# Optimization experiments

Hardware: AMD Instinct MI355X
Metric: run time of the kernel (lower is better)

The kernel has to match this reference:

```python
import jax, jax.numpy as jnp
import numpy as np

B, N, D, H, DA, DL = 8, 1024, 512, 8, 64, 64
U_DIM = DL * H * 3          # 1536: u channel (3 attention channels worth)
NB = 128                    # timestamp-delta buckets
HID = 4 * D                 # FFN hidden (ffn_multiply=4)
EPS = 1e-6


def _rms(x):
    return x * jax.lax.rsqrt(jnp.mean(x * x, axis=-1, keepdims=True) + EPS)


def setup_inputs() -> dict:
    key = jax.random.key(0)
    ks = jax.random.split(key, 12)
    L = N // 2
    total = B * L
    x_offsets = jnp.arange(B + 1, dtype=jnp.int32) * L
    x = jax.random.normal(ks[0], (total, D), jnp.float32)
    all_timestamps = jnp.sort(jax.random.randint(ks[1], (B, N), 0, 1_000_000, dtype=jnp.int64), axis=1)
    invalid_attn_mask = jnp.tril(jnp.ones((N, N), jnp.float32))
    uvqk = jax.random.normal(ks[2], (D, DL * H * 4 + DA * H * 2), jnp.float32) * 0.02
    pos_w = jax.random.normal(ks[3], (2 * N - 1,), jnp.float32) * 0.02
    ts_w = jax.random.normal(ks[4], (NB,), jnp.float32) * 0.02
    W0 = jax.random.normal(ks[5], (U_DIM, D), jnp.float32) * (1.0 / np.sqrt(U_DIM))
    b0 = jnp.zeros((D,), jnp.float32)
    W1 = jax.random.normal(ks[6], (D, HID), jnp.float32) * (1.0 / np.sqrt(D))
    W2 = jax.random.normal(ks[7], (HID, D), jnp.float32) * (1.0 / np.sqrt(HID))
    W3 = jax.random.normal(ks[8], (D, HID), jnp.float32) * (1.0 / np.sqrt(D))
    return dict(x=x, x_offsets=x_offsets, all_timestamps=all_timestamps,
                invalid_attn_mask=invalid_attn_mask, uvqk=uvqk, pos_w=pos_w,
                ts_w=ts_w, W0=W0, b0=b0, W1=W1, W2=W2, W3=W3)


def reference(x, x_offsets, all_timestamps, invalid_attn_mask, uvqk, pos_w, ts_w, W0, b0, W1, W2, W3):
    total = x.shape[0]
    tok = jnp.arange(total)
    b_idx = jnp.searchsorted(x_offsets, tok, side='right') - 1   # batch id per jagged token
    p_idx = tok - x_offsets[b_idx]                               # position within sequence

    # input RMSNorm + fused uvqk projection with SiLU
    normed = _rms(x)
    mm = jax.nn.silu(normed @ uvqk)
    u, v, q, k = jnp.split(mm, [U_DIM, U_DIM + DL * H, U_DIM + DL * H + DA * H], axis=1)

    def pad(vals):  # jagged_to_padded_dense
        return jnp.zeros((B, N, vals.shape[-1]), vals.dtype).at[b_idx, p_idx].set(vals)

    pq = pad(q).reshape(B, N, H, DA)
    pk = pad(k).reshape(B, N, H, DA)
    pv = pad(v).reshape(B, N, H, DL)

    # channel 1: content-content SiLU attention
    qk_attn = jax.nn.silu(jnp.einsum('bnhd,bmhd->bhnm', pq, pk)) / N
    qk_attn = qk_attn * invalid_attn_mask[None, None]

    # channel 2: relative positional bias (shared across batch)
    rel = jnp.arange(N)[:, None] - jnp.arange(N)[None, :] + (N - 1)
    pos_attn = pos_w[rel] * invalid_attn_mask                     # (N, N)

    # channel 3: log-bucketed relative temporal bias
    dt = all_timestamps[:, :, None] - all_timestamps[:, None, :]
    bucket = jnp.clip(jnp.floor(jnp.log(jnp.abs(dt).astype(jnp.float32) + 1.0)).astype(jnp.int32), 0, NB - 1)
    ts_attn = ts_w[bucket] * invalid_attn_mask[None]              # (B, N, N)

    out_pos = jnp.einsum('nm,bmhd->bnhd', pos_attn, pv)
    out_ts = jnp.einsum('bnm,bmhd->bnhd', ts_attn, pv)
    out_lat = jnp.einsum('bhnm,bmhd->bnhd', qk_attn, pv)
    combined = jnp.concatenate([out_pos, out_ts, out_lat], axis=-1).reshape(B, N, U_DIM)
    attn_output = combined[b_idx, p_idx]                          # dense_to_jagged

    # AMS gating + multistage FFN with residuals
    ams = u * _rms(attn_output)
    X = ams @ W0 + b0 + x
    nX = _rms(X)
    X1 = jax.nn.silu(nX @ W1) * (nX @ W3)
    return X1 @ W2 + X
```

## Files before the change

kernel.cpp:

```cpp
#include <hip/hip_runtime.h>
#include <hip/hip_bf16.h>
#include <cstdint>
#include <cstddef>

typedef __hip_bfloat16 bf16;
typedef __attribute__((ext_vector_type(8))) short bf8v;
typedef __attribute__((ext_vector_type(4))) float f4v;
typedef __attribute__((ext_vector_type(4))) short s4v;
typedef __attribute__((ext_vector_type(8))) short s8v;

#define DEV static __device__ __forceinline__

DEV float siluf(float v){ return v / (1.0f + __expf(-v)); }
DEV short bfs(float f){ bf16 h = __float2bfloat16(f); return __builtin_bit_cast(short, h); }
DEV float b2f(short s){ return __builtin_bit_cast(float, (unsigned)((unsigned short)s) << 16); }

DEV void gload16(const bf16* g, bf16* l){
  __builtin_amdgcn_global_load_lds((const __attribute__((address_space(1))) void*)g,
                                   (__attribute__((address_space(3))) void*)l, 16, 0, 0);
}

DEV void gemm_core128(const bf16* __restrict__ A, int lda,
                      const bf16* __restrict__ Bt, int ldb,
                      int K, bf16* As, bf16* Bs, f4v (&acc)[4][4],
                      int bm, int bn, int k0)
{
  const int t = threadIdx.x, w = t>>6, l = t&63;
  const int wr = w>>1, wc = w&1, lr = l&15, kb = l>>4;
#pragma unroll
  for (int i=0;i<4;i++)
#pragma unroll
    for (int j=0;j<4;j++) acc[i][j] = (f4v)(0.0f);

  for (int kt=k0; kt<k0+K; kt+=64){
    __syncthreads();
#pragma unroll
    for (int s=0;s<2;s++){
#pragma unroll
      for (int i=0;i<2;i++){
        int lin = t + i*256;
        gload16(A + (size_t)(bm + (lin>>2))*lda + kt + s*32 + (lin&3)*8,
                As + s*4096 + (size_t)(w*64 + i*256)*8);
      }
#pragma unroll
      for (int i=0;i<2;i++){
        int lin = t + i*256;
        gload16(Bt + (size_t)(bn + (lin>>2))*ldb + kt + s*32 + (lin&3)*8,
                Bs + s*4096 + (size_t)(w*64 + i*256)*8);
      }
    }
    __syncthreads();
#pragma unroll
    for (int s=0;s<2;s++){
      bf8v af[4], bfr[4];
#pragma unroll
      for (int i=0;i<4;i++) af[i]  = *(const bf8v*)(As + s*4096 + (wr*64 + i*16 + lr)*32 + kb*8);
#pragma unroll
      for (int j=0;j<4;j++) bfr[j] = *(const bf8v*)(Bs + s*4096 + (wc*64 + j*16 + lr)*32 + kb*8);
#pragma unroll
      for (int i=0;i<4;i++)
#pragma unroll
        for (int j=0;j<4;j++)
          acc[i][j] = __builtin_amdgcn_mfma_f32_16x16x32_bf16(af[i], bfr[j], acc[i][j], 0,0,0);
    }
  }
}

#define EPI_LOOP(...) { \
  const int t_=threadIdx.x, w_=t_>>6, l_=t_&63; \
  const int wr_=w_>>1, wc_=w_&1, lr_=l_&15, kb_=l_>>4; \
  _Pragma("unroll") for (int i_=0;i_<4;i_++) \
  _Pragma("unroll") for (int j_=0;j_<4;j_++) \
  _Pragma("unroll") for (int r_=0;r_<4;r_++){ \
    const int row = bm + wr_*64 + i_*16 + kb_*4 + r_; \
    const int col = bn + wc_*64 + j_*16 + lr_; \
    float v = acc[i_][j_][r_]; \
    __VA_ARGS__; \
  } }


__global__ __launch_bounds__(256) void k_gemm1(const bf16* __restrict__ xn,
                                               const bf16* __restrict__ uvqkT,
                                               bf16* __restrict__ mm,
                                               bf16* __restrict__ vT){
  __shared__ __align__(16) bf16 As[2*128*32];
  __shared__ __align__(16) bf16 Bs[2*128*32];
  f4v acc[4][4];
  const int bm = blockIdx.x*128, bn = blockIdx.y*128;
  gemm_core128(xn, 512, uvqkT, 512, 512, As, Bs, acc, bm, bn, 0);
  const int t=threadIdx.x, w=t>>6, l=t&63;
  const int wr=w>>1, wc=w&1, lr=l&15, kb=l>>4;
  const bool isv = (bn >= 1536) && (bn < 2048);
#pragma unroll
  for (int i=0;i<4;i++)
#pragma unroll
  for (int j=0;j<4;j++){
    const int row0 = bm + wr*64 + i*16 + kb*4;
    const int col  = bn + wc*64 + j*16 + lr;
    if (!isv){
#pragma unroll
      for (int r=0;r<4;r++)
        mm[(size_t)(row0+r)*3072 + col] = __float2bfloat16(siluf(acc[i][j][r]));
    } else {
      s4v p;
#pragma unroll
      for (int r=0;r<4;r++) p[r] = bfs(siluf(acc[i][j][r]));
      const int b = row0 >> 9, m = row0 & 511;
      *(s4v*)(vT + ((size_t)b*512 + (col-1536))*512 + m) = p;
    }
  }
}

__global__ __launch_bounds__(256) void k_attn(const bf16* __restrict__ mm,
                                              const bf16* __restrict__ vT,
                                              const bf16* __restrict__ Apos,
                                              const bf16* __restrict__ Ats,
                                              bf16* __restrict__ comb){
  __shared__ __align__(16) bf16 smem[40960];
  const int id = blockIdx.x;
  const int t = threadIdx.x, w = t>>6, l = t&63;
  const int wr = w>>1, wc = w&1, lr = l&15, kb = l>>4;

  if (id < 256){
    bf16* Qs = smem;
    bf16* Ks = smem + 8192;
    bf16* Vs = smem + 16384;
    bf16* Ss = smem + 24576;
    const int bm = (id & 3)*128;
    const int z = id >> 2, b = z>>3, h = z&7;
    const bf16* Qg = mm + (size_t)b*512*3072 + 2048 + h*64;
    const bf16* Kg = mm + (size_t)b*512*3072 + 2560 + h*64;
    const bf16* Vg = vT + ((size_t)b*512 + h*64)*512;
    f4v o[4][2];
#pragma unroll
    for (int i=0;i<4;i++)
#pragma unroll
      for (int j=0;j<2;j++) o[i][j] = (f4v)(0.0f);

#pragma unroll
    for (int p=0;p<4;p++){
      int s = t + p*256;
      gload16(Qg + (size_t)(bm + ((s>>2)&127))*3072 + (s>>9)*32 + (s&3)*8,
              Qs + (size_t)(w*64 + p*256)*8);
    }
    for (int bn=0; bn<=bm; bn+=128){
      __syncthreads();
#pragma unroll
      for (int p=0;p<4;p++){
        int s = t + p*256;
        gload16(Kg + (size_t)(bn + ((s>>2)&127))*3072 + (s>>9)*32 + (s&3)*8,
                Ks + (size_t)(w*64 + p*256)*8);
      }
#pragma unroll
      for (int p=0;p<4;p++){
        int s = t + p*256;
        gload16(Vg + (size_t)((s>>2)&63)*512 + bn + (s>>8)*32 + (s&3)*8,
                Vs + (size_t)(w*64 + p*256)*8);
      }
      __syncthreads();
      f4v sacc[4][4];
#pragma unroll
      for (int i=0;i<4;i++)
#pragma unroll
        for (int j=0;j<4;j++) sacc[i][j] = (f4v)(0.0f);
#pragma unroll
      for (int ki=0; ki<2; ki++){
        bf8v af[4], bk[4];
#pragma unroll
        for (int i=0;i<4;i++) af[i] = *(const bf8v*)(Qs + ki*4096 + (wr*64+i*16+lr)*32 + kb*8);
#pragma unroll
        for (int j=0;j<4;j++) bk[j] = *(const bf8v*)(Ks + ki*4096 + (wc*64+j*16+lr)*32 + kb*8);
#pragma unroll
        for (int i=0;i<4;i++)
#pragma unroll
          for (int j=0;j<4;j++)
            sacc[i][j] = __builtin_amdgcn_mfma_f32_16x16x32_bf16(af[i], bk[j], sacc[i][j], 0,0,0);
      }
      const bool diag = (bn == bm);
#pragma unroll
      for (int i=0;i<4;i++)
#pragma unroll
      for (int j=0;j<4;j++)
#pragma unroll
      for (int r=0;r<4;r++){
        const int row = wr*64 + i*16 + kb*4 + r;
        const int col = wc*64 + j*16 + lr;
        float sv = siluf(sacc[i][j][r])*(1.0f/1024.0f);
        if (diag && row < col) sv = 0.0f;
        Ss[(col>>5)*4096 + row*32 + (col&31)] = __float2bfloat16(sv);
      }
      __syncthreads();
#pragma unroll
      for (int kt=0; kt<4; kt++){
        bf8v af[4], bv[2];
#pragma unroll
        for (int i=0;i<4;i++) af[i] = *(const bf8v*)(Ss + kt*4096 + (wr*64+i*16+lr)*32 + kb*8);
#pragma unroll
        for (int j=0;j<2;j++) bv[j] = *(const bf8v*)(Vs + kt*2048 + (wc*32+j*16+lr)*32 + kb*8);
#pragma unroll
        for (int i=0;i<4;i++)
#pragma unroll
          for (int j=0;j<2;j++)
            o[i][j] = __builtin_amdgcn_mfma_f32_16x16x32_bf16(af[i], bv[j], o[i][j], 0,0,0);
      }
    }
#pragma unroll
    for (int i=0;i<4;i++)
#pragma unroll
    for (int j=0;j<2;j++)
#pragma unroll
    for (int r=0;r<4;r++){
      const int row = bm + wr*64 + i*16 + kb*4 + r;
      const int col = wc*32 + j*16 + lr;
      comb[((size_t)b*512 + row)*1536 + h*192 + 128 + col] = __float2bfloat16(o[i][j][r]);
    }
  } else {
    bf16* As = smem;
    bf16* Bs = smem + 8192;
    f4v acc[4][4];
    const int id2 = id - 256;
    const int bm = (id2 & 3)*128, bn = ((id2>>2)&3)*128;
    const int z = id2 >> 4, b = z>>1, ch = z&1;
    const bf16* A  = ch ? (Ats + (size_t)b*512*512) : Apos;
    const bf16* Bt = vT + (size_t)b*512*512;
    gemm_core128(A, 512, Bt, 512, bm + 128, As, Bs, acc, bm, bn, 0);
    EPI_LOOP( comb[((size_t)b*512 + row)*1536 + (col>>6)*192 + ch*64 + (col&63)]
                  = __float2bfloat16(v); )
  }
}

__global__ __launch_bounds__(256) void k_gemm_w0_sk(const bf16* __restrict__ ams,
                                                    const bf16* __restrict__ W0T,
                                                    float* __restrict__ parts){
  __shared__ __align__(16) bf16 As[2*128*32];
  __shared__ __align__(16) bf16 Bs[2*128*32];
  f4v acc[4][4];
  const int bm = blockIdx.x*128, bn = blockIdx.y*128, k0 = blockIdx.z*384;
  gemm_core128(ams, 1536, W0T, 1536, 384, As, Bs, acc, bm, bn, k0);
  float* P = parts + (size_t)blockIdx.z*4096*512;
  EPI_LOOP( P[(size_t)row*512 + col] = v; )
}

__global__ __launch_bounds__(128) void k_reduce_w0_rms(const float* __restrict__ parts,
                                                       const float* __restrict__ x,
                                                       const float* __restrict__ b0,
                                                       float* __restrict__ X,
                                                       bf16* __restrict__ nX){
  __shared__ float sbuf[16];
  const size_t row = blockIdx.x;
  const int t = threadIdx.x;
  float4 s = ((const float4*)(x + row*512))[t];
  const float4 bv = ((const float4*)b0)[t];
  s.x += bv.x; s.y += bv.y; s.z += bv.z; s.w += bv.w;
#pragma unroll
  for (int p=0;p<4;p++){
    const float4 pv = ((const float4*)(parts + (size_t)p*4096*512 + row*512))[t];
    s.x += pv.x; s.y += pv.y; s.z += pv.z; s.w += pv.w;
  }
  ((float4*)(X + row*512))[t] = s;
  float ss = s.x*s.x + s.y*s.y + s.z*s.z + s.w*s.w;
#pragma unroll
  for (int o=32;o>0;o>>=1) ss += __shfl_down(ss, o);
  const int ln = t & 63, wv = t >> 6;
  if (ln==0) sbuf[wv] = ss;
  __syncthreads();
  if (t==0) sbuf[8] = rsqrtf((sbuf[0]+sbuf[1])*(1.0f/512.0f) + 1e-6f);
  __syncthreads();
  const float r = sbuf[8];
  s4v o; o[0]=bfs(s.x*r); o[1]=bfs(s.y*r); o[2]=bfs(s.z*r); o[3]=bfs(s.w*r);
  ((s4v*)(nX + row*512))[t] = o;
}

__global__ __launch_bounds__(256) void k_gemm_w13f(const bf16* __restrict__ nX,
                                                   const bf16* __restrict__ W1T,
                                                   const bf16* __restrict__ W3T,
                                                   bf16* __restrict__ X1){
  __shared__ __align__(16) bf16 As[2*128*32];
  __shared__ __align__(16) bf16 Bs1[2*64*32];
  __shared__ __align__(16) bf16 Bs3[2*64*32];
  f4v a1[4][2], a3[4][2];
  const int bm = blockIdx.x*128, bn = blockIdx.y*64;
  const int t = threadIdx.x, w = t>>6, l = t&63;
  const int wr = w>>1, wc = w&1, lr = l&15, kb = l>>4;
#pragma unroll
  for (int i=0;i<4;i++)
#pragma unroll
    for (int j=0;j<2;j++){ a1[i][j] = (f4v)(0.0f); a3[i][j] = (f4v)(0.0f); }

  for (int kt=0; kt<512; kt+=64){
    __syncthreads();
#pragma unroll
    for (int s=0;s<2;s++){
#pragma unroll
      for (int i=0;i<2;i++){
        int lin = t + i*256;
        gload16(nX + (size_t)(bm + (lin>>2))*512 + kt + s*32 + (lin&3)*8,
                As + s*4096 + (size_t)(w*64 + i*256)*8);
      }
      gload16(W1T + (size_t)(bn + (t>>2))*512 + kt + s*32 + (t&3)*8, Bs1 + s*2048 + (size_t)(w*64)*8);
      gload16(W3T + (size_t)(bn + (t>>2))*512 + kt + s*32 + (t&3)*8, Bs3 + s*2048 + (size_t)(w*64)*8);
    }
    __syncthreads();
#pragma unroll
    for (int s=0;s<2;s++){
      bf8v af[4], b1[2], b3[2];
#pragma unroll
      for (int i=0;i<4;i++) af[i] = *(const bf8v*)(As + s*4096 + (wr*64 + i*16 + lr)*32 + kb*8);
#pragma unroll
      for (int j=0;j<2;j++){ b1[j] = *(const bf8v*)(Bs1 + s*2048 + (wc*32 + j*16 + lr)*32 + kb*8);
                             b3[j] = *(const bf8v*)(Bs3 + s*2048 + (wc*32 + j*16 + lr)*32 + kb*8); }
#pragma unroll
      for (int i=0;i<4;i++)
#pragma unroll
        for (int j=0;j<2;j++){
          a1[i][j] = __builtin_amdgcn_mfma_f32_16x16x32_bf16(af[i], b1[j], a1[i][j], 0,0,0);
          a3[i][j] = __builtin_amdgcn_mfma_f32_16x16x32_bf16(af[i], b3[j], a3[i][j], 0,0,0);
        }
    }
  }
#pragma unroll
  for (int i=0;i<4;i++)
#pragma unroll
  for (int j=0;j<2;j++)
#pragma unroll
  for (int r=0;r<4;r++){
    const int row = bm + wr*64 + i*16 + kb*4 + r;
    const int col = bn + wc*32 + j*16 + lr;
    X1[(size_t)row*2048 + col] = __float2bfloat16(siluf(a1[i][j][r]) * a3[i][j][r]);
  }
}

__global__ __launch_bounds__(256) void k_gemm_w2_sk(const bf16* __restrict__ X1,
                                                    const bf16* __restrict__ W2T,
                                                    float* __restrict__ parts){
  __shared__ __align__(16) bf16 As[2*128*32];
  __shared__ __align__(16) bf16 Bs[2*128*32];
  f4v acc[4][4];
  const int bm = blockIdx.x*128, bn = blockIdx.y*128, k0 = blockIdx.z*512;
  gemm_core128(X1, 2048, W2T, 2048, 512, As, Bs, acc, bm, bn, k0);
  float* P = parts + (size_t)blockIdx.z*4096*512;
  EPI_LOOP( P[(size_t)row*512 + col] = v; )
}

__global__ __launch_bounds__(256) void k_reduce_w2(const float* __restrict__ parts,
                                                   float* __restrict__ out){
  const int i = blockIdx.x*256 + threadIdx.x;
  float4 s = ((const float4*)out)[i];
#pragma unroll
  for (int p=0;p<4;p++){
    const float4 pv = ((const float4*)(parts + (size_t)p*4096*512))[i];
    s.x += pv.x; s.y += pv.y; s.z += pv.z; s.w += pv.w;
  }
  ((float4*)out)[i] = s;
}


__global__ __launch_bounds__(192) void k_rms_mul_u(const bf16* __restrict__ comb,
                                                   const bf16* __restrict__ mm,
                                                   bf16* __restrict__ ams){
  __shared__ float sbuf[16];
  const size_t rb = (size_t)blockIdx.x;
  const s8v cv = ((const s8v*)(comb + rb*1536))[threadIdx.x];
  float cf[8]; float ss = 0.f;
#pragma unroll
  for (int j=0;j<8;j++){ cf[j] = b2f(cv[j]); ss += cf[j]*cf[j]; }
#pragma unroll
  for (int o=32;o>0;o>>=1) ss += __shfl_down(ss, o);
  const int ln = threadIdx.x & 63, wv = threadIdx.x >> 6;
  if (ln==0) sbuf[wv] = ss;
  __syncthreads();
  if (threadIdx.x==0) sbuf[8] = rsqrtf((sbuf[0]+sbuf[1]+sbuf[2])*(1.0f/1536.0f) + 1e-6f);
  __syncthreads();
  const float r = sbuf[8];
  const s8v uv = ((const s8v*)(mm + rb*3072))[threadIdx.x];
  s8v o;
#pragma unroll
  for (int j=0;j<8;j++) o[j] = bfs(b2f(uv[j]) * cf[j] * r);
  ((s8v*)(ams + rb*1536))[threadIdx.x] = o;
}

__global__ __launch_bounds__(256) void k_prep(
    const float* __restrict__ x,    const int* __restrict__ ts,
    const float* __restrict__ pos_w,const float* __restrict__ ts_w,
    const float* __restrict__ uvqk, const float* __restrict__ W0,
    const float* __restrict__ W1,   const float* __restrict__ W3,
    const float* __restrict__ W2,
    bf16* __restrict__ xn,
    bf16* __restrict__ uvqkT, bf16* __restrict__ W0T,
    bf16* __restrict__ W13T,  bf16* __restrict__ W2T,
    bf16* __restrict__ Apos,  bf16* __restrict__ Ats){
  __shared__ float tile[32][33];
  __shared__ float sbuf[16];
  int id = blockIdx.x;
  if (id < 5376){
    const float* src; bf16* dst; int R, C;
    if      (id < 1536){            src=uvqk; dst=uvqkT;                  R=512;  C=3072; }
    else if (id < 2304){ id-=1536;  src=W0;   dst=W0T;                    R=1536; C=512;  }
    else if (id < 3328){ id-=2304;  src=W1;   dst=W13T;                   R=512;  C=2048; }
    else if (id < 4352){ id-=3328;  src=W3;   dst=W13T+(size_t)2048*512;  R=512;  C=2048; }
    else               { id-=4352;  src=W2;   dst=W2T;                    R=2048; C=512;  }
    const int nbx = C >> 5;
    const int c0 = (id % nbx)*32, r0 = (id / nbx)*32;
    const int tx = threadIdx.x & 31, ty = threadIdx.x >> 5;
#pragma unroll
    for (int i=0;i<32;i+=8) tile[ty+i][tx] = src[(size_t)(r0+ty+i)*C + (c0+tx)];
    __syncthreads();
#pragma unroll
    for (int i=0;i<32;i+=8) dst[(size_t)(c0+ty+i)*R + (r0+tx)] = __float2bfloat16(tile[tx][ty+i]);
  } else if (id < 14592){
    int id2 = id - 5376;
    const int mblk = id2 & 1, n = (id2>>1)&511, z = id2>>10;
    if (mblk*256 > n) return;
    const int m = mblk*256 + threadIdx.x;
    if (z == 0){
      float v = (n >= m) ? pos_w[n - m + 1023] : 0.f;
      Apos[(size_t)n*512 + m] = __float2bfloat16(v);
    } else {
      const int b = z-1;
      int dt = ts[b*1024 + n] - ts[b*1024 + m];
      float ad = (float)(dt < 0 ? -dt : dt);
      int bucket = (int)floorf(logf(ad + 1.0f));
      bucket = bucket < 0 ? 0 : (bucket > 127 ? 127 : bucket);
      float v = (n >= m) ? ts_w[bucket] : 0.f;
      Ats[((size_t)b*512 + n)*512 + m] = __float2bfloat16(v);
    }
  } else {
    const size_t row = id - 14592;
    const int t = threadIdx.x;
    if (t >= 128) return;
    const float4 v = ((const float4*)(x + row*512))[t];
    float ss = v.x*v.x + v.y*v.y + v.z*v.z + v.w*v.w;
#pragma unroll
    for (int o=32;o>0;o>>=1) ss += __shfl_down(ss, o);
    const int ln = t & 63, wv = t >> 6;
    if (ln==0) sbuf[wv] = ss;
    __syncthreads();
    if (t==0) sbuf[8] = rsqrtf((sbuf[0]+sbuf[1])*(1.0f/512.0f) + 1e-6f);
    __syncthreads();
    const float r = sbuf[8];
    s4v o; o[0]=bfs(v.x*r); o[1]=bfs(v.y*r); o[2]=bfs(v.z*r); o[3]=bfs(v.w*r);
    ((s4v*)(xn + row*512))[t] = o;
  }
}


extern "C" void kernel_launch(void* const* d_in, const int* in_sizes, int n_in,
                              void* d_out, int out_size, void* d_ws, size_t ws_size,
                              hipStream_t stream) {
  const float* x     = (const float*)d_in[0];
  const int*   ts    = (const int*)d_in[2];
  const float* uvqk  = (const float*)d_in[4];
  const float* pos_w = (const float*)d_in[5];
  const float* ts_w  = (const float*)d_in[6];
  const float* W0    = (const float*)d_in[7];
  const float* b0    = (const float*)d_in[8];
  const float* W1    = (const float*)d_in[9];
  const float* W2    = (const float*)d_in[10];
  const float* W3    = (const float*)d_in[11];
  float* out = (float*)d_out;

  char* w = (char*)d_ws;
  auto alloc = [&](size_t bytes){ char* p = w; w += (bytes + 255) & ~(size_t)255; return p; };
  bf16*  xn    = (bf16*)alloc((size_t)4096*512*2);
  bf16*  uvqkT = (bf16*)alloc((size_t)3072*512*2);
  bf16*  W0T   = (bf16*)alloc((size_t)512*1536*2);
  bf16*  W13T  = (bf16*)alloc((size_t)4096*512*2);
  bf16*  W2T   = (bf16*)alloc((size_t)512*2048*2);
  bf16*  mm    = (bf16*)alloc((size_t)4096*3072*2);
  bf16*  vT    = (bf16*)alloc((size_t)8*512*512*2);
  bf16*  Apos  = (bf16*)alloc((size_t)512*512*2);
  bf16*  Ats   = (bf16*)alloc((size_t)8*512*512*2);
  bf16*  X1    = (bf16*)alloc((size_t)4096*2048*2);
  bf16*  comb  = (bf16*)alloc((size_t)4096*1536*2);
  bf16*  ams   = (bf16*)alloc((size_t)4096*1536*2);
  bf16*  nX    = (bf16*)alloc((size_t)4096*512*2);
  float* parts = (float*)alloc((size_t)4*4096*512*4);

  k_prep<<<18688, 256, 0, stream>>>(x, ts, pos_w, ts_w, uvqk, W0, W1, W3, W2,
                                    xn, uvqkT, W0T, W13T, W2T, Apos, Ats);
  k_gemm1<<<dim3(32, 24), 256, 0, stream>>>(xn, uvqkT, mm, vT);
  k_attn<<<512, 256, 0, stream>>>(mm, vT, Apos, Ats, comb);
  k_rms_mul_u<<<4096, 192, 0, stream>>>(comb, mm, ams);
  k_gemm_w0_sk<<<dim3(32, 4, 4), 256, 0, stream>>>(ams, W0T, parts);
  k_reduce_w0_rms<<<4096, 128, 0, stream>>>(parts, x, b0, out, nX);
  k_gemm_w13f<<<dim3(32, 32), 256, 0, stream>>>(nX, W13T, W13T + (size_t)2048*512, X1);
  k_gemm_w2_sk<<<dim3(32, 4, 4), 256, 0, stream>>>(X1, W2T, parts);
  k_reduce_w2<<<2048, 256, 0, stream>>>(parts, out);
}
```

Baseline: 152.0 us.

## Overlap weight transposes and bias-table builds with the uvqk GEMM

Splits the prep kernel so only the xn normalization and uvqk transpose run before the first GEMM. The remaining weight transposes (W0, W1, W3, W2) and the Apos/Ats bias-table construction move into extra blocks of the same launch as the uvqk GEMM, so those independent memory-bound jobs share the GPU with the GEMM's compute-bound tiles. It also reverses the row-block order of the positional/timestamp GEMM blocks in the attention kernel, so the longest causal tiles start first. The cost is that the fused launch now uses a 32 KB shared-memory footprint for every block, including the small transpose blocks, which may lower occupancy for them.

```diff
diff --git a/kernel.cpp b/kernel.cpp
--- a/kernel.cpp
+++ b/kernel.cpp
@@ -78,337 +78,96 @@
     __VA_ARGS__; \
   } }
 
-
-__global__ __launch_bounds__(256) void k_gemm1(const bf16* __restrict__ xn,
-                                               const bf16* __restrict__ uvqkT,
-                                               bf16* __restrict__ mm,
-                                               bf16* __restrict__ vT){
-  __shared__ __align__(16) bf16 As[2*128*32];
-  __shared__ __align__(16) bf16 Bs[2*128*32];
-  f4v acc[4][4];
-  const int bm = blockIdx.x*128, bn = blockIdx.y*128;
-  gemm_core128(xn, 512, uvqkT, 512, 512, As, Bs, acc, bm, bn, 0);
-  const int t=threadIdx.x, w=t>>6, l=t&63;
-  const int wr=w>>1, wc=w&1, lr=l&15, kb=l>>4;
-  const bool isv = (bn >= 1536) && (bn < 2048);
-#pragma unroll
-  for (int i=0;i<4;i++)
-#pragma unroll
-  for (int j=0;j<4;j++){
-    const int row0 = bm + wr*64 + i*16 + kb*4;
-    const int col  = bn + wc*64 + j*16 + lr;
-    if (!isv){
-#pragma unroll
-      for (int r=0;r<4;r++)
-        mm[(size_t)(row0+r)*3072 + col] = __float2bfloat16(siluf(acc[i][j][r]));
-    } else {
-      s4v p;
-#pragma unroll
-      for (int r=0;r<4;r++) p[r] = bfs(siluf(acc[i][j][r]));
-      const int b = row0 >> 9, m = row0 & 511;
-      *(s4v*)(vT + ((size_t)b*512 + (col-1536))*512 + m) = p;
-    }
-  }
-}
-
-__global__ __launch_bounds__(256) void k_attn(const bf16* __restrict__ mm,
-                                              const bf16* __restrict__ vT,
-                                              const bf16* __restrict__ Apos,
-                                              const bf16* __restrict__ Ats,
-                                              bf16* __restrict__ comb){
-  __shared__ __align__(16) bf16 smem[40960];
-  const int id = blockIdx.x;
-  const int t = threadIdx.x, w = t>>6, l = t&63;
-  const int wr = w>>1, wc = w&1, lr = l&15, kb = l>>4;
-
-  if (id < 256){
-    bf16* Qs = smem;
-    bf16* Ks = smem + 8192;
-    bf16* Vs = smem + 16384;
-    bf16* Ss = smem + 24576;
-    const int bm = (id & 3)*128;
-    const int z = id >> 2, b = z>>3, h = z&7;
-    const bf16* Qg = mm + (size_t)b*512*3072 + 2048 + h*64;
-    const bf16* Kg = mm + (size_t)b*512*3072 + 2560 + h*64;
-    const bf16* Vg = vT + ((size_t)b*512 + h*64)*512;
-    f4v o[4][2];
-#pragma unroll
-    for (int i=0;i<4;i++)
-#pragma unroll
-      for (int j=0;j<2;j++) o[i][j] = (f4v)(0.0f);
-
-#pragma unroll
-    for (int p=0;p<4;p++){
-      int s = t + p*256;
-      gload16(Qg + (size_t)(bm + ((s>>2)&127))*3072 + (s>>9)*32 + (s&3)*8,
-              Qs + (size_t)(w*64 + p*256)*8);
-    }
-    for (int bn=0; bn<=bm; bn+=128){
-      __syncthreads();
-#pragma unroll
-      for (int p=0;p<4;p++){
-        int s = t + p*256;
-        gload16(Kg + (size_t)(bn + ((s>>2)&127))*3072 + (s>>9)*32 + (s&3)*8,
-                Ks + (size_t)(w*64 + p*256)*8);
-      }
-#pragma unroll
-      for (int p=0;p<4;p++){
-        int s = t + p*256;
-        gload16(Vg + (size_t)((s>>2)&63)*512 + bn + (s>>8)*32 + (s&3)*8,
-                Vs + (size_t)(w*64 + p*256)*8);
-      }
-      __syncthreads();
-      f4v sacc[4][4];
-#pragma unroll
-      for (int i=0;i<4;i++)
-#pragma unroll
-        for (int j=0;j<4;j++) sacc[i][j] = (f4v)(0.0f);
-#pragma unroll
-      for (int ki=0; ki<2; ki++){
-        bf8v af[4], bk[4];
-#pragma unroll
-        for (int i=0;i<4;i++) af[i] = *(const bf8v*)(Qs + ki*4096 + (wr*64+i*16+lr)*32 + kb*8);
-#pragma unroll
-        for (int j=0;j<4;j++) bk[j] = *(const bf8v*)(Ks + ki*4096 + (wc*64+j*16+lr)*32 + kb*8);
-#pragma unroll
-        for (int i=0;i<4;i++)
-#pragma unroll
-          for (int j=0;j<4;j++)
-            sacc[i][j] = __builtin_amdgcn_mfma_f32_16x16x32_bf16(af[i], bk[j], sacc[i][j], 0,0,0);
-      }
-      const bool diag = (bn == bm);
-#pragma unroll
-      for (int i=0;i<4;i++)
-#pragma unroll
-      for (int j=0;j<4;j++)
-#pragma unroll
-      for (int r=0;r<4;r++){
-        const int row = wr*64 + i*16 + kb*4 + r;
-        const int col = wc*64 + j*16 + lr;
-        float sv = siluf(sacc[i][j][r])*(1.0f/1024.0f);
-        if (diag && row < col) sv = 0.0f;
-        Ss[(col>>5)*4096 + row*32 + (col&31)] = __float2bfloat16(sv);
-      }
-      __syncthreads();
-#pragma unroll
-      for (int kt=0; kt<4; kt++){
-        bf8v af[4], bv[2];
-#pragma unroll
-        for (int i=0;i<4;i++) af[i] = *(const bf8v*)(Ss + kt*4096 + (wr*64+i*16+lr)*32 + kb*8);
-#pragma unroll
-        for (int j=0;j<2;j++) bv[j] = *(const bf8v*)(Vs + kt*2048 + (wc*32+j*16+lr)*32 + kb*8);
-#pragma unroll
-        for (int i=0;i<4;i++)
-#pragma unroll
-          for (int j=0;j<2;j++)
-            o[i][j] = __builtin_amdgcn_mfma_f32_16x16x32_bf16(af[i], bv[j], o[i][j], 0,0,0);
-      }
-    }
-#pragma unroll
-    for (int i=0;i<4;i++)
-#pragma unroll
-    for (int j=0;j<2;j++)
-#pragma unroll
-    for (int r=0;r<4;r++){
-      const int row = bm + wr*64 + i*16 + kb*4 + r;
-      const int col = wc*32 + j*16 + lr;
-      comb[((size_t)b*512 + row)*1536 + h*192 + 128 + col] = __float2bfloat16(o[i][j][r]);
-    }
-  } else {
-    bf16* As = smem;
-    bf16* Bs = smem + 8192;
-    f4v acc[4][4];
-    const int id2 = id - 256;
-    const int bm = (id2 & 3)*128, bn = ((id2>>2)&3)*128;
-    const int z = id2 >> 4, b = z>>1, ch = z&1;
-    const bf16* A  = ch ? (Ats + (size_t)b*512*512) : Apos;
-    const bf16* Bt = vT + (size_t)b*512*512;
-    gemm_core128(A, 512, Bt, 512, bm + 128, As, Bs, acc, bm, bn, 0);
-    EPI_LOOP( comb[((size_t)b*512 + row)*1536 + (col>>6)*192 + ch*64 + (col&63)]
-                  = __float2bfloat16(v); )
-  }
-}
-
-__global__ __launch_bounds__(256) void k_gemm_w0_sk(const bf16* __restrict__ ams,
-                                                    const bf16* __restrict__ W0T,
-                                                    float* __restrict__ parts){
-  __shared__ __align__(16) bf16 As[2*128*32];
-  __shared__ __align__(16) bf16 Bs[2*128*32];
-  f4v acc[4][4];
-  const int bm = blockIdx.x*128, bn = blockIdx.y*128, k0 = blockIdx.z*384;
-  gemm_core128(ams, 1536, W0T, 1536, 384, As, Bs, acc, bm, bn, k0);
-  float* P = parts + (size_t)blockIdx.z*4096*512;
-  EPI_LOOP( P[(size_t)row*512 + col] = v; )
-}
-
-__global__ __launch_bounds__(128) void k_reduce_w0_rms(const float* __restrict__ parts,
-                                                       const float* __restrict__ x,
-                                                       const float* __restrict__ b0,
-                                                       float* __restrict__ X,
-                                                       bf16* __restrict__ nX){
-  __shared__ float sbuf[16];
-  const size_t row = blockIdx.x;
-  const int t = threadIdx.x;
-  float4 s = ((const float4*)(x + row*512))[t];
-  const float4 bv = ((const float4*)b0)[t];
-  s.x += bv.x; s.y += bv.y; s.z += bv.z; s.w += bv.w;
-#pragma unroll
-  for (int p=0;p<4;p++){
-    const float4 pv = ((const float4*)(parts + (size_t)p*4096*512 + row*512))[t];
-    s.x += pv.x; s.y += pv.y; s.z += pv.z; s.w += pv.w;
-  }
-  ((float4*)(X + row*512))[t] = s;
-  float ss = s.x*s.x + s.y*s.y + s.z*s.z + s.w*s.w;
-#pragma unroll
-  for (int o=32;o>0;o>>=1) ss += __shfl_down(ss, o);
-  const int ln = t & 63, wv = t >> 6;
-  if (ln==0) sbuf[wv] = ss;
-  __syncthreads();
-  if (t==0) sbuf[8] = rsqrtf((sbuf[0]+sbuf[1])*(1.0f/512.0f) + 1e-6f);
-  __syncthreads();
-  const float r = sbuf[8];
-  s4v o; o[0]=bfs(s.x*r); o[1]=bfs(s.y*r); o[2]=bfs(s.z*r); o[3]=bfs(s.w*r);
-  ((s4v*)(nX + row*512))[t] = o;
-}
-
-__global__ __launch_bounds__(256) void k_gemm_w13f(const bf16* __restrict__ nX,
-                                                   const bf16* __restrict__ W1T,
-                                                   const bf16* __restrict__ W3T,
-                                                   bf16* __restrict__ X1){
-  __shared__ __align__(16) bf16 As[2*128*32];
-  __shared__ __align__(16) bf16 Bs1[2*64*32];
-  __shared__ __align__(16) bf16 Bs3[2*64*32];
-  f4v a1[4][2], a3[4][2];
-  const int bm = blockIdx.x*128, bn = blockIdx.y*64;
-  const int t = threadIdx.x, w = t>>6, l = t&63;
-  const int wr = w>>1, wc = w&1, lr = l&15, kb = l>>4;
-#pragma unroll
-  for (int i=0;i<4;i++)
-#pragma unroll
-    for (int j=0;j<2;j++){ a1[i][j] = (f4v)(0.0f); a3[i][j] = (f4v)(0.0f); }
-
-  for (int kt=0; kt<512; kt+=64){
-    __syncthreads();
-#pragma unroll
-    for (int s=0;s<2;s++){
-#pragma unroll
-      for (int i=0;i<2;i++){
-        int lin = t + i*256;
-        gload16(nX + (size_t)(bm + (lin>>2))*512 + kt + s*32 + (lin&3)*8,
-                As + s*4096 + (size_t)(w*64 + i*256)*8);
-      }
-      gload16(W1T + (size_t)(bn + (t>>2))*512 + kt + s*32 + (t&3)*8, Bs1 + s*2048 + (size_t)(w*64)*8);
-      gload16(W3T + (size_t)(bn + (t>>2))*512 + kt + s*32 + (t&3)*8, Bs3 + s*2048 + (size_t)(w*64)*8);
-    }
-    __syncthreads();
-#pragma unroll
-    for (int s=0;s<2;s++){
-      bf8v af[4], b1[2], b3[2];
-#pragma unroll
-      for (int i=0;i<4;i++) af[i] = *(const bf8v*)(As + s*4096 + (wr*64 + i*16 + lr)*32 + kb*8);
-#pragma unroll
-      for (int j=0;j<2;j++){ b1[j] = *(const bf8v*)(Bs1 + s*2048 + (wc*32 + j*16 + lr)*32 + kb*8);
-                             b3[j] = *(const bf8v*)(Bs3 + s*2048 + (wc*32 + j*16 + lr)*32 + kb*8); }
-#pragma unroll
-      for (int i=0;i<4;i++)
-#pragma unroll
-        for (int j=0;j<2;j++){
-          a1[i][j] = __builtin_amdgcn_mfma_f32_16x16x32_bf16(af[i], b1[j], a1[i][j], 0,0,0);
-          a3[i][j] = __builtin_amdgcn_mfma_f32_16x16x32_bf16(af[i], b3[j], a3[i][j], 0,0,0);
-        }
-    }
-  }
-#pragma unroll
-  for (int i=0;i<4;i++)
-#pragma unroll
-  for (int j=0;j<2;j++)
-#pragma unroll
-  for (int r=0;r<4;r++){
-    const int row = bm + wr*64 + i*16 + kb*4 + r;
-    const int col = bn + wc*32 + j*16 + lr;
-    X1[(size_t)row*2048 + col] = __float2bfloat16(siluf(a1[i][j][r]) * a3[i][j][r]);
-  }
-}
-
-__global__ __launch_bounds__(256) void k_gemm_w2_sk(const bf16* __restrict__ X1,
-                                                    const bf16* __restrict__ W2T,
-                                                    float* __restrict__ parts){
-  __shared__ __align__(16) bf16 As[2*128*32];
-  __shared__ __align__(16) bf16 Bs[2*128*32];
-  f4v acc[4][4];
-  const int bm = blockIdx.x*128, bn = blockIdx.y*128, k0 = blockIdx.z*512;
-  gemm_core128(X1, 2048, W2T, 2048, 512, As, Bs, acc, bm, bn, k0);
-  float* P = parts + (size_t)blockIdx.z*4096*512;
-  EPI_LOOP( P[(size_t)row*512 + col] = v; )
-}
-
-__global__ __launch_bounds__(256) void k_reduce_w2(const float* __restrict__ parts,
-                                                   float* __restrict__ out){
-  const int i = blockIdx.x*256 + threadIdx.x;
-  float4 s = ((const float4*)out)[i];
-#pragma unroll
-  for (int p=0;p<4;p++){
-    const float4 pv = ((const float4*)(parts + (size_t)p*4096*512))[i];
-    s.x += pv.x; s.y += pv.y; s.z += pv.z; s.w += pv.w;
-  }
-  ((float4*)out)[i] = s;
-}
-
-
-__global__ __launch_bounds__(192) void k_rms_mul_u(const bf16* __restrict__ comb,
-                                                   const bf16* __restrict__ mm,
-                                                   bf16* __restrict__ ams){
-  __shared__ float sbuf[16];
-  const size_t rb = (size_t)blockIdx.x;
-  const s8v cv = ((const s8v*)(comb + rb*1536))[threadIdx.x];
-  float cf[8]; float ss = 0.f;
-#pragma unroll
-  for (int j=0;j<8;j++){ cf[j] = b2f(cv[j]); ss += cf[j]*cf[j]; }
-#pragma unroll
-  for (int o=32;o>0;o>>=1) ss += __shfl_down(ss, o);
-  const int ln = threadIdx.x & 63, wv = threadIdx.x >> 6;
-  if (ln==0) sbuf[wv] = ss;
-  __syncthreads();
-  if (threadIdx.x==0) sbuf[8] = rsqrtf((sbuf[0]+sbuf[1]+sbuf[2])*(1.0f/1536.0f) + 1e-6f);
-  __syncthreads();
-  const float r = sbuf[8];
-  const s8v uv = ((const s8v*)(mm + rb*3072))[threadIdx.x];
-  s8v o;
-#pragma unroll
-  for (int j=0;j<8;j++) o[j] = bfs(b2f(uv[j]) * cf[j] * r);
-  ((s8v*)(ams + rb*1536))[threadIdx.x] = o;
-}
-
-__global__ __launch_bounds__(256) void k_prep(
-    const float* __restrict__ x,    const int* __restrict__ ts,
-    const float* __restrict__ pos_w,const float* __restrict__ ts_w,
-    const float* __restrict__ uvqk, const float* __restrict__ W0,
-    const float* __restrict__ W1,   const float* __restrict__ W3,
-    const float* __restrict__ W2,
-    bf16* __restrict__ xn,
-    bf16* __restrict__ uvqkT, bf16* __restrict__ W0T,
-    bf16* __restrict__ W13T,  bf16* __restrict__ W2T,
-    bf16* __restrict__ Apos,  bf16* __restrict__ Ats){
+__global__ __launch_bounds__(256) void k_pre(
+    const float* __restrict__ x, const float* __restrict__ uvqk,
+    bf16* __restrict__ xn, bf16* __restrict__ uvqkT){
   __shared__ float tile[32][33];
   __shared__ float sbuf[16];
   int id = blockIdx.x;
-  if (id < 5376){
-    const float* src; bf16* dst; int R, C;
-    if      (id < 1536){            src=uvqk; dst=uvqkT;                  R=512;  C=3072; }
-    else if (id < 2304){ id-=1536;  src=W0;   dst=W0T;                    R=1536; C=512;  }
-    else if (id < 3328){ id-=2304;  src=W1;   dst=W13T;                   R=512;  C=2048; }
-    else if (id < 4352){ id-=3328;  src=W3;   dst=W13T+(size_t)2048*512;  R=512;  C=2048; }
-    else               { id-=4352;  src=W2;   dst=W2T;                    R=2048; C=512;  }
-    const int nbx = C >> 5;
+  if (id < 1536){
+    const int nbx = 96;
     const int c0 = (id % nbx)*32, r0 = (id / nbx)*32;
     const int tx = threadIdx.x & 31, ty = threadIdx.x >> 5;
 #pragma unroll
+    for (int i=0;i<32;i+=8) tile[ty+i][tx] = uvqk[(size_t)(r0+ty+i)*3072 + (c0+tx)];
+    __syncthreads();
+#pragma unroll
+    for (int i=0;i<32;i+=8) uvqkT[(size_t)(c0+ty+i)*512 + (r0+tx)] = __float2bfloat16(tile[tx][ty+i]);
+  } else {
+    const size_t row = id - 1536;
+    const int t = threadIdx.x;
+    if (t >= 128) return;
+    const float4 v = ((const float4*)(x + row*512))[t];
+    float ss = v.x*v.x + v.y*v.y + v.z*v.z + v.w*v.w;
+#pragma unroll
+    for (int o=32;o>0;o>>=1) ss += __shfl_down(ss, o);
+    const int ln = t & 63, wv = t >> 6;
+    if (ln==0) sbuf[wv] = ss;
+    __syncthreads();
+    if (t==0) sbuf[8] = rsqrtf((sbuf[0]+sbuf[1])*(1.0f/512.0f) + 1e-6f);
+    __syncthreads();
+    const float r = sbuf[8];
+    s4v o; o[0]=bfs(v.x*r); o[1]=bfs(v.y*r); o[2]=bfs(v.z*r); o[3]=bfs(v.w*r);
+    ((s4v*)(xn + row*512))[t] = o;
+  }
+}
+
+__global__ __launch_bounds__(256) void k_gemm1x(
+    const bf16* __restrict__ xn,   const bf16* __restrict__ uvqkT,
+    const int* __restrict__ ts,    const float* __restrict__ pos_w,
+    const float* __restrict__ ts_w,
+    const float* __restrict__ W0,  const float* __restrict__ W1,
+    const float* __restrict__ W3,  const float* __restrict__ W2,
+    bf16* __restrict__ mm,  bf16* __restrict__ vT,
+    bf16* __restrict__ W0T, bf16* __restrict__ W13T, bf16* __restrict__ W2T,
+    bf16* __restrict__ Apos, bf16* __restrict__ Ats){
+  __shared__ __align__(16) char smem_raw[32768];
+  int id = blockIdx.x;
+  if (id < 768){
+    bf16* As = (bf16*)smem_raw;
+    bf16* Bs = (bf16*)(smem_raw + 16384);
+    f4v acc[4][4];
+    const int bm = (id & 31)*128, bn = (id >> 5)*128;
+    gemm_core128(xn, 512, uvqkT, 512, 512, As, Bs, acc, bm, bn, 0);
+    const int t=threadIdx.x, w=t>>6, l=t&63;
+    const int wr=w>>1, wc=w&1, lr=l&15, kb=l>>4;
+    const bool isv = (bn >= 1536) && (bn < 2048);
+#pragma unroll
+    for (int i=0;i<4;i++)
+#pragma unroll
+    for (int j=0;j<4;j++){
+      const int row0 = bm + wr*64 + i*16 + kb*4;
+      const int col  = bn + wc*64 + j*16 + lr;
+      if (!isv){
+#pragma unroll
+        for (int r=0;r<4;r++)
+          mm[(size_t)(row0+r)*3072 + col] = __float2bfloat16(siluf(acc[i][j][r]));
+      } else {
+        s4v p;
+#pragma unroll
+        for (int r=0;r<4;r++) p[r] = bfs(siluf(acc[i][j][r]));
+        const int b = row0 >> 9, m = row0 & 511;
+        *(s4v*)(vT + ((size_t)b*512 + (col-1536))*512 + m) = p;
+      }
+    }
+  } else if (id < 4608){
+    int id2 = id - 768;
+    const float* src; bf16* dst; int R, C;
+    if      (id2 < 768){             src=W0; dst=W0T;                    R=1536; C=512;  }
+    else if (id2 < 1792){ id2-=768;  src=W1; dst=W13T;                   R=512;  C=2048; }
+    else if (id2 < 2816){ id2-=1792; src=W3; dst=W13T+(size_t)2048*512;  R=512;  C=2048; }
+    else                { id2-=2816; src=W2; dst=W2T;                    R=2048; C=512;  }
+    float (*tile)[33] = (float(*)[33])smem_raw;
+    const int nbx = C >> 5;
+    const int c0 = (id2 % nbx)*32, r0 = (id2 / nbx)*32;
+    const int tx = threadIdx.x & 31, ty = threadIdx.x >> 5;
+#pragma unroll
     for (int i=0;i<32;i+=8) tile[ty+i][tx] = src[(size_t)(r0+ty+i)*C + (c0+tx)];
     __syncthreads();
 #pragma unroll
     for (int i=0;i<32;i+=8) dst[(size_t)(c0+ty+i)*R + (r0+tx)] = __float2bfloat16(tile[tx][ty+i]);
-  } else if (id < 14592){
-    int id2 = id - 5376;
+  } else {
+    int id2 = id - 4608;
     const int mblk = id2 & 1, n = (id2>>1)&511, z = id2>>10;
     if (mblk*256 > n) return;
     const int m = mblk*256 + threadIdx.x;
@@ -424,23 +183,275 @@
       float v = (n >= m) ? ts_w[bucket] : 0.f;
       Ats[((size_t)b*512 + n)*512 + m] = __float2bfloat16(v);
     }
+  }
+}
+
+__global__ __launch_bounds__(256) void k_attn(const bf16* __restrict__ mm,
+                                              const bf16* __restrict__ vT,
+                                              const bf16* __restrict__ Apos,
+                                              const bf16* __restrict__ Ats,
+                                              bf16* __restrict__ comb){
+  __shared__ __align__(16) bf16 smem[40960];
+  const int id = blockIdx.x;
+  const int t = threadIdx.x, w = t>>6, l = t&63;
+  const int wr = w>>1, wc = w&1, lr = l&15, kb = l>>4;
+
+  if (id < 256){
+    bf16* Qs = smem;
+    bf16* Ks = smem + 8192;
+    bf16* Vs = smem + 16384;
+    bf16* Ss = smem + 24576;
+    const int bm = (3-(id & 3))*128;
+    const int z = id >> 2, b = z>>3, h = z&7;
+    const bf16* Qg = mm + (size_t)b*512*3072 + 2048 + h*64;
+    const bf16* Kg = mm + (size_t)b*512*3072 + 2560 + h*64;
+    const bf16* Vg = vT + ((size_t)b*512 + h*64)*512;
+    f4v o[4][2];
+#pragma unroll
+    for (int i=0;i<4;i++)
+#pragma unroll
+      for (int j=0;j<2;j++) o[i][j] = (f4v)(0.0f);
+
+#pragma unroll
+    for (int p=0;p<4;p++){
+      int s = t + p*256;
+      gload16(Qg + (size_t)(bm + ((s>>2)&127))*3072 + (s>>9)*32 + (s&3)*8,
+              Qs + (size_t)(w*64 + p*256)*8);
+    }
+    for (int bn=0; bn<=bm; bn+=128){
+      __syncthreads();
+#pragma unroll
+      for (int p=0;p<4;p++){
+        int s = t + p*256;
+        gload16(Kg + (size_t)(bn + ((s>>2)&127))*3072 + (s>>9)*32 + (s&3)*8,
+                Ks + (size_t)(w*64 + p*256)*8);
+      }
+#pragma unroll
+      for (int p=0;p<4;p++){
+        int s = t + p*256;
+        gload16(Vg + (size_t)((s>>2)&63)*512 + bn + (s>>8)*32 + (s&3)*8,
+                Vs + (size_t)(w*64 + p*256)*8);
+      }
+      __syncthreads();
+      f4v sacc[4][4];
+#pragma unroll
+      for (int i=0;i<4;i++)
+#pragma unroll
+        for (int j=0;j<4;j++) sacc[i][j] = (f4v)(0.0f);
+#pragma unroll
+      for (int ki=0; ki<2; ki++){
+        bf8v af[4], bk[4];
+#pragma unroll
+        for (int i=0;i<4;i++) af[i] = *(const bf8v*)(Qs + ki*4096 + (wr*64+i*16+lr)*32 + kb*8);
+#pragma unroll
+        for (int j=0;j<4;j++) bk[j] = *(const bf8v*)(Ks + ki*4096 + (wc*64+j*16+lr)*32 + kb*8);
+#pragma unroll
+        for (int i=0;i<4;i++)
+#pragma unroll
+          for (int j=0;j<4;j++)
+            sacc[i][j] = __builtin_amdgcn_mfma_f32_16x16x32_bf16(af[i], bk[j], sacc[i][j], 0,0,0);
+      }
+      const bool diag = (bn == bm);
+#pragma unroll
+      for (int i=0;i<4;i++)
+#pragma unroll
+      for (int j=0;j<4;j++)
+#pragma unroll
+      for (int r=0;r<4;r++){
+        const int row = wr*64 + i*16 + kb*4 + r;
+        const int col = wc*64 + j*16 + lr;
+        float sv = siluf(sacc[i][j][r])*(1.0f/1024.0f);
+        if (diag && row < col) sv = 0.0f;
+        Ss[(col>>5)*4096 + row*32 + (col&31)] = __float2bfloat16(sv);
+      }
+      __syncthreads();
+#pragma unroll
+      for (int kt=0; kt<4; kt++){
+        bf8v af[4], bv[2];
+#pragma unroll
+        for (int i=0;i<4;i++) af[i] = *(const bf8v*)(Ss + kt*4096 + (wr*64+i*16+lr)*32 + kb*8);
+#pragma unroll
+        for (int j=0;j<2;j++) bv[j] = *(const bf8v*)(Vs + kt*2048 + (wc*32+j*16+lr)*32 + kb*8);
+#pragma unroll
+        for (int i=0;i<4;i++)
+#pragma unroll
+          for (int j=0;j<2;j++)
+            o[i][j] = __builtin_amdgcn_mfma_f32_16x16x32_bf16(af[i], bv[j], o[i][j], 0,0,0);
+      }
+    }
+#pragma unroll
+    for (int i=0;i<4;i++)
+#pragma unroll
+    for (int j=0;j<2;j++)
+#pragma unroll
+    for (int r=0;r<4;r++){
+      const int row = bm + wr*64 + i*16 + kb*4 + r;
+      const int col = wc*32 + j*16 + lr;
+      comb[((size_t)b*512 + row)*1536 + h*192 + 128 + col] = __float2bfloat16(o[i][j][r]);
+    }
   } else {
-    const size_t row = id - 14592;
-    const int t = threadIdx.x;
-    if (t >= 128) return;
-    const float4 v = ((const float4*)(x + row*512))[t];
-    float ss = v.x*v.x + v.y*v.y + v.z*v.z + v.w*v.w;
-#pragma unroll
-    for (int o=32;o>0;o>>=1) ss += __shfl_down(ss, o);
-    const int ln = t & 63, wv = t >> 6;
-    if (ln==0) sbuf[wv] = ss;
-    __syncthreads();
-    if (t==0) sbuf[8] = rsqrtf((sbuf[0]+sbuf[1])*(1.0f/512.0f) + 1e-6f);
-    __syncthreads();
-    const float r = sbuf[8];
-    s4v o; o[0]=bfs(v.x*r); o[1]=bfs(v.y*r); o[2]=bfs(v.z*r); o[3]=bfs(v.w*r);
-    ((s4v*)(xn + row*512))[t] = o;
-  }
+    bf16* As = smem;
+    bf16* Bs = smem + 8192;
+    f4v acc[4][4];
+    const int id2 = id - 256;
+    const int bm = (3-(id2 & 3))*128, bn = ((id2>>2)&3)*128;
+    const int z = id2 >> 4, b = z>>1, ch = z&1;
+    const bf16* A  = ch ? (Ats + (size_t)b*512*512) : Apos;
+    const bf16* Bt = vT + (size_t)b*512*512;
+    gemm_core128(A, 512, Bt, 512, bm + 128, As, Bs, acc, bm, bn, 0);
+    EPI_LOOP( comb[((size_t)b*512 + row)*1536 + (col>>6)*192 + ch*64 + (col&63)]
+                  = __float2bfloat16(v); )
+  }
+}
+
+__global__ __launch_bounds__(256) void k_gemm_w0_sk(const bf16* __restrict__ ams,
+                                                    const bf16* __restrict__ W0T,
+                                                    float* __restrict__ parts){
+  __shared__ __align__(16) bf16 As[2*128*32];
+  __shared__ __align__(16) bf16 Bs[2*128*32];
+  f4v acc[4][4];
+  const int bm = blockIdx.x*128, bn = blockIdx.y*128, k0 = blockIdx.z*384;
+  gemm_core128(ams, 1536, W0T, 1536, 384, As, Bs, acc, bm, bn, k0);
+  float* P = parts + (size_t)blockIdx.z*4096*512;
+  EPI_LOOP( P[(size_t)row*512 + col] = v; )
+}
+
+__global__ __launch_bounds__(128) void k_reduce_w0_rms(const float* __restrict__ parts,
+                                                       const float* __restrict__ x,
+                                                       const float* __restrict__ b0,
+                                                       float* __restrict__ X,
+                                                       bf16* __restrict__ nX){
+  __shared__ float sbuf[16];
+  const size_t row = blockIdx.x;
+  const int t = threadIdx.x;
+  float4 s = ((const float4*)(x + row*512))[t];
+  const float4 bv = ((const float4*)b0)[t];
+  s.x += bv.x; s.y += bv.y; s.z += bv.z; s.w += bv.w;
+#pragma unroll
+  for (int p=0;p<4;p++){
+    const float4 pv = ((const float4*)(parts + (size_t)p*4096*512 + row*512))[t];
+    s.x += pv.x; s.y += pv.y; s.z += pv.z; s.w += pv.w;
+  }
+  ((float4*)(X + row*512))[t] = s;
+  float ss = s.x*s.x + s.y*s.y + s.z*s.z + s.w*s.w;
+#pragma unroll
+  for (int o=32;o>0;o>>=1) ss += __shfl_down(ss, o);
+  const int ln = t & 63, wv = t >> 6;
+  if (ln==0) sbuf[wv] = ss;
+  __syncthreads();
+  if (t==0) sbuf[8] = rsqrtf((sbuf[0]+sbuf[1])*(1.0f/512.0f) + 1e-6f);
+  __syncthreads();
+  const float r = sbuf[8];
+  s4v o; o[0]=bfs(s.x*r); o[1]=bfs(s.y*r); o[2]=bfs(s.z*r); o[3]=bfs(s.w*r);
+  ((s4v*)(nX + row*512))[t] = o;
+}
+
+__global__ __launch_bounds__(256) void k_gemm_w13f(const bf16* __restrict__ nX,
+                                                   const bf16* __restrict__ W1T,
+                                                   const bf16* __restrict__ W3T,
+                                                   bf16* __restrict__ X1){
+  __shared__ __align__(16) bf16 As[2*128*32];
+  __shared__ __align__(16) bf16 Bs1[2*64*32];
+  __shared__ __align__(16) bf16 Bs3[2*64*32];
+  f4v a1[4][2], a3[4][2];
+  const int bm = blockIdx.x*128, bn = blockIdx.y*64;
+  const int t = threadIdx.x, w = t>>6, l = t&63;
+  const int wr = w>>1, wc = w&1, lr = l&15, kb = l>>4;
+#pragma unroll
+  for (int i=0;i<4;i++)
+#pragma unroll
+    for (int j=0;j<2;j++){ a1[i][j] = (f4v)(0.0f); a3[i][j] = (f4v)(0.0f); }
+
+  for (int kt=0; kt<512; kt+=64){
+    __syncthreads();
+#pragma unroll
+    for (int s=0;s<2;s++){
+#pragma unroll
+      for (int i=0;i<2;i++){
+        int lin = t + i*256;
+        gload16(nX + (size_t)(bm + (lin>>2))*512 + kt + s*32 + (lin&3)*8,
+                As + s*4096 + (size_t)(w*64 + i*256)*8);
+      }
+      gload16(W1T + (size_t)(bn + (t>>2))*512 + kt + s*32 + (t&3)*8, Bs1 + s*2048 + (size_t)(w*64)*8);
+      gload16(W3T + (size_t)(bn + (t>>2))*512 + kt + s*32 + (t&3)*8, Bs3 + s*2048 + (size_t)(w*64)*8);
+    }
+    __syncthreads();
+#pragma unroll
+    for (int s=0;s<2;s++){
+      bf8v af[4], b1[2], b3[2];
+#pragma unroll
+      for (int i=0;i<4;i++) af[i] = *(const bf8v*)(As + s*4096 + (wr*64 + i*16 + lr)*32 + kb*8);
+#pragma unroll
+      for (int j=0;j<2;j++){ b1[j] = *(const bf8v*)(Bs1 + s*2048 + (wc*32 + j*16 + lr)*32 + kb*8);
+                             b3[j] = *(const bf8v*)(Bs3 + s*2048 + (wc*32 + j*16 + lr)*32 + kb*8); }
+#pragma unroll
+      for (int i=0;i<4;i++)
+#pragma unroll
+        for (int j=0;j<2;j++){
+          a1[i][j] = __builtin_amdgcn_mfma_f32_16x16x32_bf16(af[i], b1[j], a1[i][j], 0,0,0);
+          a3[i][j] = __builtin_amdgcn_mfma_f32_16x16x32_bf16(af[i], b3[j], a3[i][j], 0,0,0);
+        }
+    }
+  }
+#pragma unroll
+  for (int i=0;i<4;i++)
+#pragma unroll
+  for (int j=0;j<2;j++)
+#pragma unroll
+  for (int r=0;r<4;r++){
+    const int row = bm + wr*64 + i*16 + kb*4 + r;
+    const int col = bn + wc*32 + j*16 + lr;
+    X1[(size_t)row*2048 + col] = __float2bfloat16(siluf(a1[i][j][r]) * a3[i][j][r]);
+  }
+}
+
+__global__ __launch_bounds__(256) void k_gemm_w2_sk(const bf16* __restrict__ X1,
+                                                    const bf16* __restrict__ W2T,
+                                                    float* __restrict__ parts){
+  __shared__ __align__(16) bf16 As[2*128*32];
+  __shared__ __align__(16) bf16 Bs[2*128*32];
+  f4v acc[4][4];
+  const int bm = blockIdx.x*128, bn = blockIdx.y*128, k0 = blockIdx.z*512;
+  gemm_core128(X1, 2048, W2T, 2048, 512, As, Bs, acc, bm, bn, k0);
+  float* P = parts + (size_t)blockIdx.z*4096*512;
+  EPI_LOOP( P[(size_t)row*512 + col] = v; )
+}
+
+__global__ __launch_bounds__(256) void k_reduce_w2(const float* __restrict__ parts,
+                                                   float* __restrict__ out){
+  const int i = blockIdx.x*256 + threadIdx.x;
+  float4 s = ((const float4*)out)[i];
+#pragma unroll
+  for (int p=0;p<4;p++){
+    const float4 pv = ((const float4*)(parts + (size_t)p*4096*512))[i];
+    s.x += pv.x; s.y += pv.y; s.z += pv.z; s.w += pv.w;
+  }
+  ((float4*)out)[i] = s;
+}
+
+
+__global__ __launch_bounds__(192) void k_rms_mul_u(const bf16* __restrict__ comb,
+                                                   const bf16* __restrict__ mm,
+                                                   bf16* __restrict__ ams){
+  __shared__ float sbuf[16];
+  const size_t rb = (size_t)blockIdx.x;
+  const s8v cv = ((const s8v*)(comb + rb*1536))[threadIdx.x];
+  float cf[8]; float ss = 0.f;
+#pragma unroll
+  for (int j=0;j<8;j++){ cf[j] = b2f(cv[j]); ss += cf[j]*cf[j]; }
+#pragma unroll
+  for (int o=32;o>0;o>>=1) ss += __shfl_down(ss, o);
+  const int ln = threadIdx.x & 63, wv = threadIdx.x >> 6;
+  if (ln==0) sbuf[wv] = ss;
+  __syncthreads();
+  if (threadIdx.x==0) sbuf[8] = rsqrtf((sbuf[0]+sbuf[1]+sbuf[2])*(1.0f/1536.0f) + 1e-6f);
+  __syncthreads();
+  const float r = sbuf[8];
+  const s8v uv = ((const s8v*)(mm + rb*3072))[threadIdx.x];
+  s8v o;
+#pragma unroll
+  for (int j=0;j<8;j++) o[j] = bfs(b2f(uv[j]) * cf[j] * r);
+  ((s8v*)(ams + rb*1536))[threadIdx.x] = o;
 }
 
 
@@ -476,9 +487,9 @@
   bf16*  nX    = (bf16*)alloc((size_t)4096*512*2);
   float* parts = (float*)alloc((size_t)4*4096*512*4);
 
-  k_prep<<<18688, 256, 0, stream>>>(x, ts, pos_w, ts_w, uvqk, W0, W1, W3, W2,
-                                    xn, uvqkT, W0T, W13T, W2T, Apos, Ats);
-  k_gemm1<<<dim3(32, 24), 256, 0, stream>>>(xn, uvqkT, mm, vT);
+  k_pre<<<5632, 256, 0, stream>>>(x, uvqk, xn, uvqkT);
+  k_gemm1x<<<13824, 256, 0, stream>>>(xn, uvqkT, ts, pos_w, ts_w, W0, W1, W3, W2,
+                                      mm, vT, W0T, W13T, W2T, Apos, Ats);
   k_attn<<<512, 256, 0, stream>>>(mm, vT, Apos, Ats, comb);
   k_rms_mul_u<<<4096, 192, 0, stream>>>(comb, mm, ams);
   k_gemm_w0_sk<<<dim3(32, 4, 4), 256, 0, stream>>>(ams, W0T, parts);
```

New measurement: 158.8 us. 4.5% more time.
